# Optimization experiments

Hardware: AMD Instinct MI355X
Metric: run time of the kernel (lower is better)

Reference implementation:

```python
import jax, jax.numpy as jnp
import numpy as np

B, T, D = 4, 2048, 1024  # batch, seq_len, dec_dim_in == dim_proj_QK == dim_proj_V == dec_dim_out


def setup_inputs() -> dict:
    key = jax.random.key(0)
    ks = jax.random.split(key, 9)
    s = 1.0 / np.sqrt(D)  # torch Linear default init scale
    return {
        "x": jax.random.normal(ks[0], (B, T, D), dtype=jnp.float32),
        "Wq": jax.random.uniform(ks[1], (D, D), jnp.float32, -s, s),
        "bq": jax.random.uniform(ks[2], (D,), jnp.float32, -s, s),
        "Wk": jax.random.uniform(ks[3], (D, D), jnp.float32, -s, s),
        "bk": jax.random.uniform(ks[4], (D,), jnp.float32, -s, s),
        "Wv": jax.random.uniform(ks[5], (D, D), jnp.float32, -s, s),
        "bv": jax.random.uniform(ks[6], (D,), jnp.float32, -s, s),
        "Wh": jax.random.uniform(ks[7], (D, D), jnp.float32, -s, s),
        "bh": jax.random.uniform(ks[8], (D,), jnp.float32, -s, s),
    }


def reference(x, Wq, bq, Wk, bk, Wv, bv, Wh, bh):
    Q = x @ Wq + bq                      # [B, T, Dqk]
    K = x @ Wk + bk                      # [B, T, Dqk]
    V = x @ Wv + bv                      # [B, T, Dv]
    scale = 1.0 / jnp.sqrt(jnp.asarray(K.shape[-1], x.dtype))
    scores = jnp.einsum("btd,bsd->bts", Q, K) * scale  # [B, T, T]
    t = K.shape[1]
    causal = jnp.triu(jnp.ones((t, t), dtype=bool), k=1)  # True above diagonal
    scores = jnp.where(causal[None, :, :], -jnp.inf, scores)
    attn = jax.nn.softmax(scores, axis=-1)
    # dropout is identity in eval mode (reference baseline)
    out = jnp.einsum("bts,bsd->btd", attn, V)  # [B, T, Dv]
    return out @ Wh + bh
```

## Files before the change

### kernel.cpp

```cpp
#include <hip/hip_runtime.h>


typedef __attribute__((ext_vector_type(8)))  short short8;
typedef __attribute__((ext_vector_type(4)))  float f4;

#define BM 128
#define BN 128
#define BK 64
#define BM2 256
#define BN2 256

#define F_OBF    1
#define F_SKIP   2
#define F_KLIM   4
#define F_REVY   8
#define F_VSPL   16
#define F_RSCL   32
#define F_EXP    64
#define F_RSUM   128
#define F_SPLITK 256

#define WAITV4() asm volatile("s_waitcnt vmcnt(4)" ::: "memory")
#define WAITV8() asm volatile("s_waitcnt vmcnt(8)" ::: "memory")
#define WAITV0() asm volatile("s_waitcnt vmcnt(0)" ::: "memory")
#define SBAR()   __builtin_amdgcn_s_barrier()
#define PRIO1()  __builtin_amdgcn_s_setprio(1)
#define PRIO0()  __builtin_amdgcn_s_setprio(0)

__device__ inline unsigned short f2bf(float f) {
    union { float f; unsigned u; } c; c.f = f;
    unsigned u = c.u;
    return (unsigned short)((u + 0x7fffu + ((u >> 16) & 1u)) >> 16);
}
__device__ inline float bf2f(unsigned short u) {
    union { unsigned u; float f; } c; c.u = ((unsigned)u) << 16;
    return c.f;
}
__device__ inline void gload16(const void* g, void* l) {
    __builtin_amdgcn_global_load_lds(
        (const __attribute__((address_space(1))) void*)g,
        (__attribute__((address_space(3))) void*)l,
        16, 0, 0);
}

template<int FLAGS>
__global__ __launch_bounds__(256)
void gemm_bt(const unsigned short* __restrict__ A,
             const unsigned short* __restrict__ Bt,
             void* __restrict__ C,
             const float* __restrict__ bias,
             int M, int N, int K, int lda, int ldb, int ldc,
             long sA, long sB, long sC,
             float scale,
             unsigned short* __restrict__ C2, long sC2, int Tv, int vsplit,
             float* __restrict__ rowsums)
{
    const int b = blockIdx.z;
    A  += (long)b * sA;
    Bt += (long)b * sB;

    int by = blockIdx.y;
    if (FLAGS & F_REVY) by = gridDim.y - 1 - by;
    const int m0 = by * BM;
    const int n0 = blockIdx.x * BN;

    const int kt1 = K / BK;

    __shared__ unsigned short As[BM * BK];
    __shared__ unsigned short Bs[BN * BK];

    const int tid  = threadIdx.x;
    const int lane = tid & 63;
    const int wave = tid >> 6;
    const int wm   = wave & 1;
    const int wn   = wave >> 1;
    const int lrow = lane & 15;
    const int quad = lane >> 4;

    f4 acc[4][4];
#pragma unroll
    for (int i = 0; i < 4; ++i)
#pragma unroll
        for (int j = 0; j < 4; ++j) acc[i][j] = (f4)0.0f;

    const int srow = tid >> 3;
    const int gco  = ((tid & 7) ^ (srow & 7)) << 3;
    const int rdsl = (lrow & 7);

    for (int kt = 0; kt < kt1; ++kt) {
        const int k0 = kt * BK;
#pragma unroll
        for (int d = 0; d < 4; ++d) {
            const int row = d * 32 + srow;
            const unsigned short* ga = A  + (long)(m0 + row) * lda + k0 + gco;
            const unsigned short* gb = Bt + (long)(n0 + row) * ldb + k0 + gco;
            const int ldsoff = (d * 256 + wave * 64) * 16;
            gload16(ga, (char*)As + ldsoff);
            gload16(gb, (char*)Bs + ldsoff);
        }
        __syncthreads();

#pragma unroll
        for (int ks = 0; ks < 2; ++ks) {
            const int slot = ((ks * 4 + quad) ^ rdsl) << 3;
            short8 af[4], bfr[4];
#pragma unroll
            for (int i = 0; i < 4; ++i) {
                af[i]  = *(const short8*)(As + (wm * 64 + i * 16 + lrow) * BK + slot);
                bfr[i] = *(const short8*)(Bs + (wn * 64 + i * 16 + lrow) * BK + slot);
            }
#pragma unroll
            for (int i = 0; i < 4; ++i)
#pragma unroll
                for (int j = 0; j < 4; ++j)
                    acc[i][j] = __builtin_amdgcn_mfma_f32_16x16x32_bf16(
                        af[i], bfr[j], acc[i][j], 0, 0, 0);
        }
        __syncthreads();
    }

    const int row0 = m0 + wm * 64 + quad * 4;
    const int col0 = n0 + wn * 64 + lrow;

    float bj[4];
#pragma unroll
    for (int j = 0; j < 4; ++j) bj[j] = bias ? bias[col0 + j * 16] : 0.0f;

    unsigned short* Cb = (unsigned short*)C;
    float*          Cf = (float*)C;
    const long cbase = (long)b * sC;

#pragma unroll
    for (int i = 0; i < 4; ++i) {
#pragma unroll
        for (int j = 0; j < 4; ++j) {
            const int col = col0 + j * 16;
#pragma unroll
            for (int r = 0; r < 4; ++r) {
                const int row = row0 + i * 16 + r;
                float v = acc[i][j][r] * scale + bj[j];
                const long off = cbase + (long)row * ldc + col;
                if (FLAGS & F_OBF) Cb[off] = f2bf(v);
                else               Cf[off] = v;
            }
        }
    }
}

template<int HA>
__device__ inline void lda_half(short8 (&af)[8], const unsigned short* Asb,
                                int wm, int lrow, int quad, int rdsl)
{
#pragma unroll
    for (int i = 0; i < 4; ++i)
#pragma unroll
        for (int ks = 0; ks < 2; ++ks)
            af[i * 2 + ks] = *(const short8*)(
                Asb + (wm * 128 + HA * 64 + i * 16 + lrow) * BK
                    + (((ks * 4 + quad) ^ rdsl) << 3));
}

template<int QB>
__device__ inline void ldb_q(short8 (&bq)[4], const unsigned short* Bsb,
                             int wn, int lrow, int quad, int rdsl)
{
#pragma unroll
    for (int j = 0; j < 2; ++j)
#pragma unroll
        for (int ks = 0; ks < 2; ++ks)
            bq[j * 2 + ks] = *(const short8*)(
                Bsb + (wn * 64 + QB * 32 + j * 16 + lrow) * BK
                    + (((ks * 4 + quad) ^ rdsl) << 3));
}

template<int RI, int CJ>
__device__ inline void mfma_cl(f4 (&acc)[8][4], const short8 (&a)[8],
                               const short8 (&b)[4])
{
#pragma unroll
    for (int ks = 0; ks < 2; ++ks)
#pragma unroll
        for (int i = 0; i < 4; ++i)
#pragma unroll
            for (int j = 0; j < 2; ++j)
                acc[RI + i][CJ + j] = __builtin_amdgcn_mfma_f32_16x16x32_bf16(
                    a[i * 2 + ks], b[j * 2 + ks], acc[RI + i][CJ + j], 0, 0, 0);
}

__device__ inline void stage_mat(const unsigned short* __restrict__ Row,
                                 int k0, unsigned short* Ls, int ld, int tid)
{
    const int srow = tid >> 3;
    const int gco  = ((tid & 7) ^ (srow & 7)) << 3;
    const int wave = tid >> 6;
#pragma unroll
    for (int d = 0; d < 4; ++d) {
        const int row = d * 64 + srow;
        const int ldsoff = (d * 512 + wave * 64) * 16;
        gload16(Row + (long)row * ld + k0 + gco, (char*)Ls + ldsoff);
    }
}

template<int FLAGS, int GX = 0, int GY = 0>
__global__ __launch_bounds__(512)
void gemm256(const unsigned short* __restrict__ A,
             const unsigned short* __restrict__ Bt,
             void* __restrict__ C,
             const float* __restrict__ bias,
             int M, int N, int K, int lda, int ldb, int ldc,
             long sA, long sB, long sC,
             float scale,
             unsigned short* __restrict__ C2, long sC2, int Tv, int vsplit,
             float* __restrict__ rowsums)
{
    const int b = blockIdx.z;
    A  += (long)b * sA;
    Bt += (long)b * sB;
    if (FLAGS & (F_RSCL | F_RSUM)) rowsums += (long)b * M;

    int bxr = blockIdx.x, byr = blockIdx.y;
    if (GX > 0) {
        constexpr int NWG = GX * GY;
        constexpr int Q   = NWG >> 3;
        static_assert((NWG & 7) == 0, "swizzle needs NWG%8==0");
        const int lin  = byr * GX + bxr;
        const int virt = (lin & 7) * Q + (lin >> 3);
        bxr = virt % GX; byr = virt / GX;
    }

    int by = byr;
    if (FLAGS & F_REVY) by = gridDim.y - 1 - by;
    const int m0 = by * BM2;

    int n0, split = 0;
    if (FLAGS & F_SPLITK) {
        const int nbx = N / BN2;
        n0 = (bxr % nbx) * BN2;
        split = bxr / nbx;
        if (split && m0 < 1024) return;
    } else {
        n0 = bxr * BN2;
    }

    if ((FLAGS & F_SKIP) && n0 > m0 + (BM2 - 1)) return;

    int kend = K;
    if (FLAGS & F_KLIM) { int ke = m0 + BM2; kend = ke < K ? ke : K; }
    int kt0 = 0;
    if (FLAGS & F_SPLITK) {
        if (split == 0) { if (kend > 1024) kend = 1024; }
        else            { kt0 = 1024 / BK; }
    }
    const int kt1 = kend / BK;

    __shared__ unsigned short sm[4][BM2 * BK];

    const int tid  = threadIdx.x;
    const int lane = tid & 63;
    const int wave = tid >> 6;
    const int wm   = wave & 1;
    const int wn   = wave >> 1;
    const int lrow = lane & 15;
    const int quad = lane >> 4;
    const int rdsl = lrow & 7;

    f4 acc[8][4];
#pragma unroll
    for (int i = 0; i < 8; ++i)
#pragma unroll
        for (int j = 0; j < 4; ++j) acc[i][j] = (f4)0.0f;

    const unsigned short* Arow = A  + (long)m0 * lda;
    const unsigned short* Brow = Bt + (long)n0 * ldb;
    const int ktiles = kt1 - kt0;

    short8 af[8], bg0[4], bg1[4];

    stage_mat(Arow, kt0 * BK, sm[0], lda, tid);
    stage_mat(Brow, kt0 * BK, sm[1], ldb, tid);
    stage_mat(Arow, (kt0 + 1) * BK, sm[2], lda, tid);
    stage_mat(Brow, (kt0 + 1) * BK, sm[3], ldb, tid);
    WAITV8();
    SBAR();
    lda_half<0>(af, sm[0], wm, lrow, quad, rdsl);
    ldb_q<0>(bg0, sm[1], wn, lrow, quad, rdsl);

    for (int t = 0; t < ktiles; ++t) {
        const int cur = t & 1;
        const unsigned short* Asb = sm[cur * 2];
        const unsigned short* Bsb = sm[cur * 2 + 1];
        const bool s2 = (t + 2 < ktiles);
        const bool rd = (t + 1 < ktiles);

        PRIO1(); mfma_cl<0, 0>(acc, af, bg0); PRIO0();
        ldb_q<1>(bg1, Bsb, wn, lrow, quad, rdsl);
        SBAR();

        PRIO1(); mfma_cl<0, 2>(acc, af, bg1); PRIO0();
        lda_half<1>(af, Asb, wm, lrow, quad, rdsl);
        SBAR();

        PRIO1(); mfma_cl<4, 2>(acc, af, bg1); PRIO0();
        if (s2) { stage_mat(Arow, (kt0 + t + 2) * BK, sm[cur * 2], lda, tid);
                  WAITV4(); }
        else    { WAITV0(); }
        SBAR();

        if (s2) stage_mat(Brow, (kt0 + t + 2) * BK, sm[cur * 2 + 1], ldb, tid);
        PRIO1(); mfma_cl<4, 0>(acc, af, bg0); PRIO0();
        if (rd) {
            const unsigned short* An = sm[(cur ^ 1) * 2];
            const unsigned short* Bn = sm[(cur ^ 1) * 2 + 1];
            lda_half<0>(af, An, wm, lrow, quad, rdsl);
            ldb_q<0>(bg0, Bn, wn, lrow, quad, rdsl);
        }
        SBAR();
    }

    const int row0 = m0 + wm * 128 + quad * 4;
    const int col0 = n0 + wn * 64 + lrow;

    float bj[4];
#pragma unroll
    for (int j = 0; j < 4; ++j) bj[j] = bias ? bias[col0 + j * 16] : 0.0f;

    if ((FLAGS & F_VSPL) && n0 >= vsplit) {
        const int bidx  = m0 >> 11;
        const int tloc0 = (m0 & 2047) + wm * 128 + quad * 4;
#pragma unroll
        for (int j = 0; j < 4; ++j) {
            const int d = col0 + j * 16 - vsplit;
            unsigned short* base = C2 + (long)bidx * sC2 + (long)d * Tv;
#pragma unroll
            for (int i = 0; i < 8; ++i) {
                const int tt = tloc0 + i * 16;
                unsigned long long pk = 0;
#pragma unroll
                for (int r = 0; r < 4; ++r) {
                    float v = acc[i][j][r] * scale + bj[j];
                    pk |= (unsigned long long)f2bf(v) << (16 * r);
                }
                *(unsigned long long*)(base + tt) = pk;
            }
        }
        return;
    }

    float inv[32];
    if (FLAGS & F_RSCL) {
#pragma unroll
        for (int i = 0; i < 8; ++i)
#pragma unroll
            for (int r = 0; r < 4; ++r)
                inv[i * 4 + r] = rowsums[row0 + i * 16 + r];
    }

    float rs[32];
    if (FLAGS & F_RSUM) {
#pragma unroll
        for (int k = 0; k < 32; ++k) rs[k] = 0.0f;
    }

    unsigned short* Cb = (unsigned short*)C;
    float*          Cf = ((FLAGS & F_SPLITK) && split) ? (float*)C2 : (float*)C;
    const long cbase = (long)b * sC;

#pragma unroll
    for (int i = 0; i < 8; ++i) {
#pragma unroll
        for (int j = 0; j < 4; ++j) {
            const int col = col0 + j * 16;
#pragma unroll
            for (int r = 0; r < 4; ++r) {
                const int row = row0 + i * 16 + r;
                float v = acc[i][j][r] * scale;
                if (FLAGS & F_EXP) { v = __expf(v); if (col > row) v = 0.0f; }
                if (FLAGS & F_RSUM) rs[i * 4 + r] += v;
                if (FLAGS & F_RSCL) v *= inv[i * 4 + r];
                if (!((FLAGS & F_SPLITK) && split)) v += bj[j];
                const long off = cbase + (long)row * ldc + col;
                if (FLAGS & F_OBF) Cb[off] = f2bf(v);
                else               Cf[off] = v;
            }
        }
    }

    if (FLAGS & F_RSUM) {
#pragma unroll
        for (int k = 0; k < 32; ++k) {
            rs[k] += __shfl_xor(rs[k], 1);
            rs[k] += __shfl_xor(rs[k], 2);
            rs[k] += __shfl_xor(rs[k], 4);
            rs[k] += __shfl_xor(rs[k], 8);
        }
        if (lrow == 0) {
#pragma unroll
            for (int i = 0; i < 8; ++i)
#pragma unroll
                for (int r = 0; r < 4; ++r)
                    atomicAdd(&rowsums[row0 + i * 16 + r], rs[i * 4 + r]);
        }
    }
}

__global__ void combine_upper(float* __restrict__ out,
                              const float* __restrict__ part)
{
    const long base = ((long)blockIdx.y * 2048 + 1024) * 1024 / 4;
    const long i = base + blockIdx.x * 256 + threadIdx.x;
    f4 a = ((f4*)out)[i];
    f4 bb = ((const f4*)part)[i];
    a.x += bb.x; a.y += bb.y; a.z += bb.z; a.w += bb.w;
    ((f4*)out)[i] = a;
}

__global__ void recip_sums(float* __restrict__ s)
{
    const int i = blockIdx.x * 256 + threadIdx.x;
    s[i] = 1.0f / s[i];
}

__global__ void gemv_bhh(const unsigned short* __restrict__ Wht,
                         const float* __restrict__ bv,
                         const float* __restrict__ bh,
                         float* __restrict__ bhh)
{
    const int m = blockIdx.x;
    const int tid = threadIdx.x;
    const int lane = tid & 63, wave = tid >> 6;
    __shared__ float red[4];
    const unsigned short* row = Wht + (long)m * 1024;
    float s = 0.0f;
#pragma unroll
    for (int k = 0; k < 4; ++k) {
        const int idx = tid * 4 + k;
        s += bf2f(row[idx]) * bv[idx];
    }
    for (int o = 32; o > 0; o >>= 1) s += __shfl_down(s, o);
    if (lane == 0) red[wave] = s;
    __syncthreads();
    if (tid == 0) bhh[m] = red[0] + red[1] + red[2] + red[3] + bh[m];
}

__global__ void prep(const float* __restrict__ x,
                     const float* __restrict__ Wq, const float* __restrict__ Wk,
                     const float* __restrict__ Wv, const float* __restrict__ Wh,
                     const float* __restrict__ bq, const float* __restrict__ bk,
                     unsigned short* __restrict__ Xbf,
                     unsigned short* __restrict__ Wqkvt,
                     unsigned short* __restrict__ Wht,
                     unsigned short* __restrict__ Wvb,
                     float* __restrict__ bqkv)
{
    __shared__ unsigned short tsh[32][33];
    const int bid = blockIdx.x;
    const int tid = threadIdx.x;

    if (bid < 8192) {
        const int i = bid * 256 + tid;
        f4 v = ((const f4*)x)[i];
        unsigned long long p = (unsigned long long)f2bf(v.x)
                             | ((unsigned long long)f2bf(v.y) << 16)
                             | ((unsigned long long)f2bf(v.z) << 32)
                             | ((unsigned long long)f2bf(v.w) << 48);
        ((unsigned long long*)Xbf)[i] = p;
    } else if (bid < 9216) {
        const int i = (bid - 8192) * 256 + tid;
        f4 v = ((const f4*)Wv)[i];
        unsigned long long p = (unsigned long long)f2bf(v.x)
                             | ((unsigned long long)f2bf(v.y) << 16)
                             | ((unsigned long long)f2bf(v.z) << 32)
                             | ((unsigned long long)f2bf(v.w) << 48);
        ((unsigned long long*)Wvb)[i] = p;
    } else if (bid < 12288) {
        const int wi = bid - 9216;
        const int w = wi >> 10, tile = wi & 1023;
        const float* src = (w == 0) ? Wq : (w == 1) ? Wk : Wh;
        unsigned short* dst = (w == 0) ? Wqkvt : (w == 1) ? (Wqkvt + 1024 * 1024) : Wht;
        const int c0 = (tile & 31) * 32, r0 = (tile >> 5) * 32;
        const int xx = tid & 31, yy = tid >> 5;
        for (int i = yy; i < 32; i += 8)
            tsh[i][xx] = f2bf(src[(long)(r0 + i) * 1024 + c0 + xx]);
        __syncthreads();
        for (int i = yy; i < 32; i += 8)
            dst[(long)(c0 + i) * 1024 + r0 + xx] = tsh[xx][i];
    } else {
        const int i = (bid - 12288) * 256 + tid;
        if (i < 1024) { bqkv[i] = bq[i]; bqkv[1024 + i] = bk[i]; bqkv[2048 + i] = 0.0f; }
    }
}

extern "C" void kernel_launch(void* const* d_in, const int* in_sizes, int n_in,
                              void* d_out, int out_size, void* d_ws, size_t ws_size,
                              hipStream_t stream)
{
    const float* x  = (const float*)d_in[0];
    const float* Wq = (const float*)d_in[1];
    const float* bq = (const float*)d_in[2];
    const float* Wk = (const float*)d_in[3];
    const float* bk = (const float*)d_in[4];
    const float* Wv = (const float*)d_in[5];
    const float* bv = (const float*)d_in[6];
    const float* Wh = (const float*)d_in[7];
    const float* bh = (const float*)d_in[8];
    float* out = (float*)d_out;

    const int  Bb = 4, T = 2048, Dm = 1024;
    const long BT = (long)Bb * T;

    unsigned short* ws = (unsigned short*)d_ws;
    size_t o = 0;
    unsigned short* Xbf   = ws + o; o += (size_t)BT * Dm;
    unsigned short* Wqkvt = ws + o; o += (size_t)3 * Dm * Dm;
    unsigned short* Wht   = ws + o; o += (size_t)Dm * Dm;
    unsigned short* Wvb   = ws + o; o += (size_t)Dm * Dm;
    float* bqkv = (float*)(ws + o); o += (size_t)3 * Dm * 2;
    float* bhh  = (float*)(ws + o); o += (size_t)Dm * 2;
    float* sums = (float*)(ws + o); o += (size_t)BT * 2;
    unsigned short* QKV   = ws + o; o += (size_t)BT * 3 * Dm;
    unsigned short* Vt    = ws + o; o += (size_t)BT * Dm;
    unsigned short* Pp    = ws + o; o += (size_t)Bb * T * T;
    float* part = (float*)(ws + o);

    const dim3 blk(256);
    const dim3 blk2(512);
    const long sRow3 = (long)T * 3 * Dm;

    hipMemsetAsync(sums, 0, (size_t)BT * sizeof(float), stream);

    prep<<<12289, blk, 0, stream>>>(x, Wq, Wk, Wv, Wh, bq, bk,
                                    Xbf, Wqkvt, Wht, Wvb, bqkv);

    gemm_bt<F_OBF><<<dim3(Dm / BN, Dm / BM, 1), blk, 0, stream>>>(
        Wht, Wvb, Wqkvt + 2 * Dm * Dm, nullptr, Dm, Dm, Dm, Dm, Dm, Dm,
        0, 0, 0, 1.0f, nullptr, 0, 0, 0, nullptr);

    gemv_bhh<<<Dm, blk, 0, stream>>>(Wht, bv, bh, bhh);

    gemm256<F_OBF | F_VSPL, 12, 32>
        <<<dim3(3 * Dm / BN2, BT / BM2, 1), blk2, 0, stream>>>(
        Xbf, Wqkvt, QKV, bqkv, (int)BT, 3 * Dm, Dm, Dm, Dm, 3 * Dm,
        0, 0, 0, 1.0f, Vt, (long)Dm * T, T, 2 * Dm, nullptr);

    gemm256<F_OBF | F_SKIP | F_REVY | F_EXP | F_RSUM, 8, 8>
        <<<dim3(T / BN2, T / BM2, Bb), blk2, 0, stream>>>(
        QKV, QKV + Dm, Pp, nullptr, T, T, Dm, 3 * Dm, 3 * Dm, T,
        sRow3, sRow3, (long)T * T, 1.0f / 32.0f,
        nullptr, 0, 0, 0, sums);

    recip_sums<<<dim3((int)(BT / 256)), blk, 0, stream>>>(sums);

    gemm256<F_KLIM | F_REVY | F_RSCL | F_SPLITK, 8, 8>
        <<<dim3(2 * Dm / BN2, T / BM2, Bb), blk2, 0, stream>>>(
        Pp, Vt, out, bhh, T, Dm, T, T, T, Dm,
        (long)T * T, (long)Dm * T, (long)T * Dm, 1.0f,
        (unsigned short*)part, 0, 0, 0, sums);

    combine_upper<<<dim3(1024, Bb), blk, 0, stream>>>(out, part);
}
```

Measured before the change: 278.6 us.

## Split QKV projection into QK GEMM and separate V GEMM with 128x256 tiles

```diff
diff --git a/kernel.cpp b/kernel.cpp
--- a/kernel.cpp
+++ b/kernel.cpp
@@ -9,6 +9,8 @@
 #define BK 64
 #define BM2 256
 #define BN2 256
+#define BM3 128
+#define BN3 256
 
 #define F_OBF    1
 #define F_SKIP   2
@@ -21,6 +23,7 @@
 #define F_SPLITK 256
 
 #define WAITV4() asm volatile("s_waitcnt vmcnt(4)" ::: "memory")
+#define WAITV6() asm volatile("s_waitcnt vmcnt(6)" ::: "memory")
 #define WAITV8() asm volatile("s_waitcnt vmcnt(8)" ::: "memory")
 #define WAITV0() asm volatile("s_waitcnt vmcnt(0)" ::: "memory")
 #define SBAR()   __builtin_amdgcn_s_barrier()
@@ -147,6 +150,34 @@
     }
 }
 
+template<int QB>
+__device__ inline void ldb_q(short8 (&bq)[4], const unsigned short* Bsb,
+                             int wn, int lrow, int quad, int rdsl)
+{
+#pragma unroll
+    for (int j = 0; j < 2; ++j)
+#pragma unroll
+        for (int ks = 0; ks < 2; ++ks)
+            bq[j * 2 + ks] = *(const short8*)(
+                Bsb + (wn * 64 + QB * 32 + j * 16 + lrow) * BK
+                    + (((ks * 4 + quad) ^ rdsl) << 3));
+}
+
+template<int ND>
+__device__ inline void stage_mat(const unsigned short* __restrict__ Row,
+                                 int k0, unsigned short* Ls, int ld, int tid)
+{
+    const int srow = tid >> 3;
+    const int gco  = ((tid & 7) ^ (srow & 7)) << 3;
+    const int wave = tid >> 6;
+#pragma unroll
+    for (int d = 0; d < ND; ++d) {
+        const int row = d * 64 + srow;
+        const int ldsoff = (d * 512 + wave * 64) * 16;
+        gload16(Row + (long)row * ld + k0 + gco, (char*)Ls + ldsoff);
+    }
+}
+
 template<int HA>
 __device__ inline void lda_half(short8 (&af)[8], const unsigned short* Asb,
                                 int wm, int lrow, int quad, int rdsl)
@@ -160,19 +191,6 @@
                     + (((ks * 4 + quad) ^ rdsl) << 3));
 }
 
-template<int QB>
-__device__ inline void ldb_q(short8 (&bq)[4], const unsigned short* Bsb,
-                             int wn, int lrow, int quad, int rdsl)
-{
-#pragma unroll
-    for (int j = 0; j < 2; ++j)
-#pragma unroll
-        for (int ks = 0; ks < 2; ++ks)
-            bq[j * 2 + ks] = *(const short8*)(
-                Bsb + (wn * 64 + QB * 32 + j * 16 + lrow) * BK
-                    + (((ks * 4 + quad) ^ rdsl) << 3));
-}
-
 template<int RI, int CJ>
 __device__ inline void mfma_cl(f4 (&acc)[8][4], const short8 (&a)[8],
                                const short8 (&b)[4])
@@ -187,18 +205,30 @@
                     a[i * 2 + ks], b[j * 2 + ks], acc[RI + i][CJ + j], 0, 0, 0);
 }
 
-__device__ inline void stage_mat(const unsigned short* __restrict__ Row,
-                                 int k0, unsigned short* Ls, int ld, int tid)
-{
-    const int srow = tid >> 3;
-    const int gco  = ((tid & 7) ^ (srow & 7)) << 3;
-    const int wave = tid >> 6;
-#pragma unroll
-    for (int d = 0; d < 4; ++d) {
-        const int row = d * 64 + srow;
-        const int ldsoff = (d * 512 + wave * 64) * 16;
-        gload16(Row + (long)row * ld + k0 + gco, (char*)Ls + ldsoff);
-    }
+__device__ inline void lda_w(short8 (&af)[8], const unsigned short* Asb,
+                             int wm, int lrow, int quad, int rdsl)
+{
+#pragma unroll
+    for (int i = 0; i < 4; ++i)
+#pragma unroll
+        for (int ks = 0; ks < 2; ++ks)
+            af[i * 2 + ks] = *(const short8*)(
+                Asb + (wm * 64 + i * 16 + lrow) * BK
+                    + (((ks * 4 + quad) ^ rdsl) << 3));
+}
+
+template<int CJ>
+__device__ inline void mfma16(f4 (&acc)[4][4], const short8 (&a)[8],
+                              const short8 (&b)[4])
+{
+#pragma unroll
+    for (int ks = 0; ks < 2; ++ks)
+#pragma unroll
+        for (int i = 0; i < 4; ++i)
+#pragma unroll
+            for (int j = 0; j < 2; ++j)
+                acc[i][CJ + j] = __builtin_amdgcn_mfma_f32_16x16x32_bf16(
+                    a[i * 2 + ks], b[j * 2 + ks], acc[i][CJ + j], 0, 0, 0);
 }
 
 template<int FLAGS, int GX = 0, int GY = 0>
@@ -276,10 +306,10 @@
 
     short8 af[8], bg0[4], bg1[4];
 
-    stage_mat(Arow, kt0 * BK, sm[0], lda, tid);
-    stage_mat(Brow, kt0 * BK, sm[1], ldb, tid);
-    stage_mat(Arow, (kt0 + 1) * BK, sm[2], lda, tid);
-    stage_mat(Brow, (kt0 + 1) * BK, sm[3], ldb, tid);
+    stage_mat<4>(Arow, kt0 * BK, sm[0], lda, tid);
+    stage_mat<4>(Brow, kt0 * BK, sm[1], ldb, tid);
+    stage_mat<4>(Arow, (kt0 + 1) * BK, sm[2], lda, tid);
+    stage_mat<4>(Brow, (kt0 + 1) * BK, sm[3], ldb, tid);
     WAITV8();
     SBAR();
     lda_half<0>(af, sm[0], wm, lrow, quad, rdsl);
@@ -301,12 +331,12 @@
         SBAR();
 
         PRIO1(); mfma_cl<4, 2>(acc, af, bg1); PRIO0();
-        if (s2) { stage_mat(Arow, (kt0 + t + 2) * BK, sm[cur * 2], lda, tid);
+        if (s2) { stage_mat<4>(Arow, (kt0 + t + 2) * BK, sm[cur * 2], lda, tid);
                   WAITV4(); }
         else    { WAITV0(); }
         SBAR();
 
-        if (s2) stage_mat(Brow, (kt0 + t + 2) * BK, sm[cur * 2 + 1], ldb, tid);
+        if (s2) stage_mat<4>(Brow, (kt0 + t + 2) * BK, sm[cur * 2 + 1], ldb, tid);
         PRIO1(); mfma_cl<4, 0>(acc, af, bg0); PRIO0();
         if (rd) {
             const unsigned short* An = sm[(cur ^ 1) * 2];
@@ -399,6 +429,143 @@
 #pragma unroll
                 for (int r = 0; r < 4; ++r)
                     atomicAdd(&rowsums[row0 + i * 16 + r], rs[i * 4 + r]);
+        }
+    }
+}
+
+template<int FLAGS, int GX = 0, int GY = 0>
+__global__ __launch_bounds__(512)
+void gemmw(const unsigned short* __restrict__ A,
+           const unsigned short* __restrict__ Bt,
+           void* __restrict__ C,
+           const float* __restrict__ bias,
+           int M, int N, int K, int lda, int ldb, int ldc,
+           long sA, long sB, long sC,
+           float scale,
+           unsigned short* __restrict__ C2, long sC2, int Tv, int vsplit,
+           float* __restrict__ rowsums)
+{
+    const int b = blockIdx.z;
+    A  += (long)b * sA;
+    Bt += (long)b * sB;
+
+    int bxr = blockIdx.x, byr = blockIdx.y;
+    if (GX > 0) {
+        constexpr int NWG = GX * GY;
+        constexpr int Q   = NWG >> 3;
+        static_assert((NWG & 7) == 0, "swizzle needs NWG%8==0");
+        const int lin  = byr * GX + bxr;
+        const int virt = (lin & 7) * Q + (lin >> 3);
+        bxr = virt % GX; byr = virt / GX;
+    }
+
+    const int m0 = byr * BM3;
+    const int n0 = bxr * BN3;
+    const int kt1 = K / BK;
+
+    __shared__ unsigned short smA[2][BM3 * BK];
+    __shared__ unsigned short smB[2][BN3 * BK];
+
+    const int tid  = threadIdx.x;
+    const int lane = tid & 63;
+    const int wave = tid >> 6;
+    const int wm   = wave & 1;
+    const int wn   = wave >> 1;
+    const int lrow = lane & 15;
+    const int quad = lane >> 4;
+    const int rdsl = lrow & 7;
+
+    f4 acc[4][4];
+#pragma unroll
+    for (int i = 0; i < 4; ++i)
+#pragma unroll
+        for (int j = 0; j < 4; ++j) acc[i][j] = (f4)0.0f;
+
+    const unsigned short* Arow = A  + (long)m0 * lda;
+    const unsigned short* Brow = Bt + (long)n0 * ldb;
+    const int ktiles = kt1;
+
+    short8 af[8], bg0[4], bg1[4];
+
+    stage_mat<2>(Arow, 0, smA[0], lda, tid);
+    stage_mat<4>(Brow, 0, smB[0], ldb, tid);
+    stage_mat<2>(Arow, BK, smA[1], lda, tid);
+    stage_mat<4>(Brow, BK, smB[1], ldb, tid);
+    WAITV6();
+    SBAR();
+    lda_w(af, smA[0], wm, lrow, quad, rdsl);
+    ldb_q<0>(bg0, smB[0], wn, lrow, quad, rdsl);
+
+    for (int t = 0; t < ktiles; ++t) {
+        const int cur = t & 1;
+        const bool s2 = (t + 2 < ktiles);
+        const bool rd = (t + 1 < ktiles);
+
+        PRIO1(); mfma16<0>(acc, af, bg0); PRIO0();
+        ldb_q<1>(bg1, smB[cur], wn, lrow, quad, rdsl);
+        SBAR();
+
+        PRIO1(); mfma16<2>(acc, af, bg1); PRIO0();
+        if (s2) {
+            stage_mat<2>(Arow, (t + 2) * BK, smA[cur], lda, tid);
+            stage_mat<4>(Brow, (t + 2) * BK, smB[cur], ldb, tid);
+            WAITV6();
+        } else {
+            WAITV0();
+        }
+        SBAR();
+        if (rd) {
+            lda_w(af, smA[cur ^ 1], wm, lrow, quad, rdsl);
+            ldb_q<0>(bg0, smB[cur ^ 1], wn, lrow, quad, rdsl);
+        }
+    }
+
+    const int row0 = m0 + wm * 64 + quad * 4;
+    const int col0 = n0 + wn * 64 + lrow;
+
+    float bj[4];
+#pragma unroll
+    for (int j = 0; j < 4; ++j) bj[j] = bias ? bias[col0 + j * 16] : 0.0f;
+
+    if ((FLAGS & F_VSPL) && n0 >= vsplit) {
+        const int bidx  = m0 >> 11;
+        const int tloc0 = (m0 & 2047) + wm * 64 + quad * 4;
+#pragma unroll
+        for (int j = 0; j < 4; ++j) {
+            const int d = col0 + j * 16 - vsplit;
+            unsigned short* base = C2 + (long)bidx * sC2 + (long)d * Tv;
+#pragma unroll
+            for (int i = 0; i < 4; ++i) {
+                const int tt = tloc0 + i * 16;
+                unsigned long long pk = 0;
+#pragma unroll
+                for (int r = 0; r < 4; ++r) {
+                    float v = acc[i][j][r] * scale + bj[j];
+                    pk |= (unsigned long long)f2bf(v) << (16 * r);
+                }
+                *(unsigned long long*)(base + tt) = pk;
+            }
+        }
+        return;
+    }
+
+    unsigned short* Cb = (unsigned short*)C;
+    float*          Cf = (float*)C;
+    const long cbase = (long)b * sC;
+
+#pragma unroll
+    for (int i = 0; i < 4; ++i) {
+#pragma unroll
+        for (int j = 0; j < 4; ++j) {
+            const int col = col0 + j * 16;
+#pragma unroll
+            for (int r = 0; r < 4; ++r) {
+                const int row = row0 + i * 16 + r;
+                float v = acc[i][j][r] * scale + bj[j];
+                const long off = cbase + (long)row * ldc + col;
+                if (FLAGS & F_OBF) Cb[off] = f2bf(v);
+                else               Cf[off] = v;
+            }
         }
     }
 }
@@ -537,10 +704,15 @@
 
     gemv_bhh<<<Dm, blk, 0, stream>>>(Wht, bv, bh, bhh);
 
-    gemm256<F_OBF | F_VSPL, 12, 32>
-        <<<dim3(3 * Dm / BN2, BT / BM2, 1), blk2, 0, stream>>>(
-        Xbf, Wqkvt, QKV, bqkv, (int)BT, 3 * Dm, Dm, Dm, Dm, 3 * Dm,
-        0, 0, 0, 1.0f, Vt, (long)Dm * T, T, 2 * Dm, nullptr);
+    gemm256<F_OBF, 8, 32>
+        <<<dim3(2 * Dm / BN2, BT / BM2, 1), blk2, 0, stream>>>(
+        Xbf, Wqkvt, QKV, bqkv, (int)BT, 2 * Dm, Dm, Dm, Dm, 3 * Dm,
+        0, 0, 0, 1.0f, nullptr, 0, 0, 0, nullptr);
+
+    gemmw<F_OBF | F_VSPL, 4, 64>
+        <<<dim3(Dm / BN3, BT / BM3, 1), blk2, 0, stream>>>(
+        Xbf, Wqkvt + 2 * Dm * Dm, QKV, nullptr, (int)BT, Dm, Dm, Dm, Dm, 3 * Dm,
+        0, 0, 0, 1.0f, Vt, (long)Dm * T, T, 0, nullptr);
 
     gemm256<F_OBF | F_SKIP | F_REVY | F_EXP | F_RSUM, 8, 8>
         <<<dim3(T / BN2, T / BM2, Bb), blk2, 0, stream>>>(
```

After: 274.6 us. Within noise of the previous version (-1.4%).
